# Performance work log

Measured on AMD Instinct MI355X. Metric: run time of the kernel, lower is better.

Reference implementation:

```python
import jax, jax.numpy as jnp
import numpy as np

NEG_BIG = -9e15
ALPHA = 0.2  # LeakyReLU negative slope


def setup_inputs() -> dict:
    key = jax.random.key(0)
    k1, k2, k3, k4 = jax.random.split(key, 4)
    B, N, IN, OUT = 8, 2048, 128, 64
    x = jax.random.normal(k1, (B, N, IN), dtype=jnp.float32)
    adj = jax.random.randint(k2, (B, N, N), 0, 2, dtype=jnp.int32)
    # xavier_uniform with gain=1.414
    lim_W = 1.414 * np.sqrt(6.0 / (IN + OUT))
    W = jax.random.uniform(k3, (IN, OUT), jnp.float32, -lim_W, lim_W)
    lim_a = 1.414 * np.sqrt(6.0 / (2 * OUT + 1))
    a = jax.random.uniform(k4, (2 * OUT, 1), jnp.float32, -lim_a, lim_a)
    return {"x": x, "adj": adj, "W": W, "a": a}


def reference(x, adj, W, a):
    # h: [B, N, out_dim]
    h = jnp.matmul(x, W)
    out_dim = W.shape[1]
    a1 = a[:out_dim, 0]   # applied to h_i (row / destination)
    a2 = a[out_dim:, 0]   # applied to h_j (col / source)
    # e_ij = leakyrelu(h_i . a1 + h_j . a2)  -- avoids the O(B*N*N*2d) concat
    si = jnp.einsum('bnd,d->bn', h, a1)  # [B, N]
    sj = jnp.einsum('bnd,d->bn', h, a2)  # [B, N]
    e = si[:, :, None] + sj[:, None, :]  # [B, N, N]
    e = jnp.where(e > 0, e, ALPHA * e)   # LeakyReLU
    e = jnp.where(adj > 0, e, NEG_BIG)
    attention = jax.nn.softmax(e, axis=-1)  # [B, N, N]
    # dropout p=0.0 (eval mode): identity
    h_prime = jnp.matmul(attention, h)       # [B, N, out_dim]
    return h_prime, attention
```

## Files before the change

### kernel.cpp

```cpp
#include <hip/hip_runtime.h>

#define BB 8
#define NN 2048
#define IND 128
#define OUTD 64
#define ALPHA 0.2f

typedef __attribute__((ext_vector_type(8))) short bf16x8;
typedef __attribute__((ext_vector_type(4))) float f32x4;
typedef unsigned int u32;

__global__ __launch_bounds__(256) void k1_hproj(const float* __restrict__ x,
                                                const float* __restrict__ W,
                                                const float* __restrict__ a,
                                                short* __restrict__ hT_hi,
                                                short* __restrict__ hT_lo,
                                                float* __restrict__ si,
                                                float* __restrict__ sj) {
    __shared__ float Wl[IND * OUTD];
    __shared__ float xl[16][IND];
    __shared__ float tile[16][OUTD + 1];
    int t = threadIdx.x, lane = t & 63, wave = t >> 6;

    const float4* W4 = (const float4*)W;
    float4* Wl4 = (float4*)Wl;
    #pragma unroll
    for (int q = 0; q < 8; ++q) Wl4[t + q * 256] = W4[t + q * 256];

    int row0 = blockIdx.x * 16;
    const float4* x4 = (const float4*)(x + (size_t)row0 * IND);
    float4* xl4 = (float4*)&xl[0][0];
    xl4[t] = x4[t];
    xl4[t + 256] = x4[t + 256];
    __syncthreads();

    float a1v = a[lane];
    float a2v = a[OUTD + lane];

    float acc[4] = {0.f, 0.f, 0.f, 0.f};
    int rbase = wave * 4;
    for (int k = 0; k < IND; k += 4) {
        float4 xv0 = *(const float4*)&xl[rbase + 0][k];
        float4 xv1 = *(const float4*)&xl[rbase + 1][k];
        float4 xv2 = *(const float4*)&xl[rbase + 2][k];
        float4 xv3 = *(const float4*)&xl[rbase + 3][k];
        #pragma unroll
        for (int q = 0; q < 4; ++q) {
            float w = Wl[(k + q) * OUTD + lane];
            acc[0] = fmaf(((const float*)&xv0)[q], w, acc[0]);
            acc[1] = fmaf(((const float*)&xv1)[q], w, acc[1]);
            acc[2] = fmaf(((const float*)&xv2)[q], w, acc[2]);
            acc[3] = fmaf(((const float*)&xv3)[q], w, acc[3]);
        }
    }
    #pragma unroll
    for (int rr = 0; rr < 4; ++rr) {
        size_t grow = (size_t)row0 + rbase + rr;
        tile[rbase + rr][lane] = acc[rr];
        float v1 = acc[rr] * a1v;
        float v2 = acc[rr] * a2v;
        #pragma unroll
        for (int o = 32; o; o >>= 1) {
            v1 += __shfl_xor(v1, o);
            v2 += __shfl_xor(v2, o);
        }
        if (lane == 0) { si[grow] = v1; sj[grow] = v2; }
    }
    __syncthreads();

    int d = t >> 2, kq = (t & 3) * 4;
    int b = row0 >> 11;
    int krow = (row0 & (NN - 1)) + kq;
    float v0 = tile[kq + 0][d], v1 = tile[kq + 1][d];
    float v2 = tile[kq + 2][d], v3 = tile[kq + 3][d];
    u32 b0 = __float_as_uint(v0), b1 = __float_as_uint(v1);
    u32 b2 = __float_as_uint(v2), b3 = __float_as_uint(v3);
    u32 h0 = b0 & 0xffff0000u, h1 = b1 & 0xffff0000u;
    u32 h2 = b2 & 0xffff0000u, h3 = b3 & 0xffff0000u;
    float l0 = v0 - __uint_as_float(h0), l1 = v1 - __uint_as_float(h1);
    float l2 = v2 - __uint_as_float(h2), l3 = v3 - __uint_as_float(h3);
    uint2 hi2, lo2;
    hi2.x = (b0 >> 16) | h1;
    hi2.y = (b2 >> 16) | h3;
    lo2.x = (__float_as_uint(l0) >> 16) | (__float_as_uint(l1) & 0xffff0000u);
    lo2.y = (__float_as_uint(l2) >> 16) | (__float_as_uint(l3) & 0xffff0000u);
    size_t off = ((size_t)b * OUTD + d) * NN + krow;
    *(uint2*)(hT_hi + off) = hi2;
    *(uint2*)(hT_lo + off) = lo2;
}

__global__ __launch_bounds__(256) void k2_mask(const int* __restrict__ adj,
                                               const float* __restrict__ si,
                                               const float* __restrict__ sj,
                                               float* __restrict__ invS,
                                               unsigned char* __restrict__ mask) {
    int t = threadIdx.x, lane = t & 63, w = t >> 6;
    int row = blockIdx.x * 4 + w;
    int b = row >> 11;
    float s_i = si[row];
    const int4* arow = (const int4*)(adj + (size_t)row * NN);
    const float* sjb = sj + (size_t)b * NN;

    float sum = 0.f;
    #pragma unroll
    for (int q = 0; q < 8; ++q) {
        int4 av = arow[q * 64 + lane];
        float4 sv = *(const float4*)(sjb + q * 256 + lane * 4);
        unsigned nib = 0;
        float e, pe;
        e = s_i + sv.x; e = e > 0.f ? e : ALPHA * e; pe = __expf(e);
        if (av.x > 0) { nib |= 1u; sum += pe; }
        e = s_i + sv.y; e = e > 0.f ? e : ALPHA * e; pe = __expf(e);
        if (av.y > 0) { nib |= 2u; sum += pe; }
        e = s_i + sv.z; e = e > 0.f ? e : ALPHA * e; pe = __expf(e);
        if (av.z > 0) { nib |= 4u; sum += pe; }
        e = s_i + sv.w; e = e > 0.f ? e : ALPHA * e; pe = __expf(e);
        if (av.w > 0) { nib |= 8u; sum += pe; }
        unsigned pn = (unsigned)__shfl_xor((int)nib, 1);
        if (!(lane & 1))
            mask[(size_t)row * 256 + q * 32 + (lane >> 1)] = (unsigned char)(nib | (pn << 4));
    }
    #pragma unroll
    for (int o = 32; o; o >>= 1) sum += __shfl_xor(sum, o);
    if (lane == 0) invS[row] = sum > 0.f ? 1.0f / sum : 0.f;
}

__global__ __launch_bounds__(256) void k3_attn_pv(const unsigned char* __restrict__ mask,
                                                  const float* __restrict__ si,
                                                  const float* __restrict__ sj,
                                                  const float* __restrict__ invS,
                                                  const short* __restrict__ hT_hi,
                                                  const short* __restrict__ hT_lo,
                                                  float* __restrict__ attn,
                                                  float* __restrict__ hp) {
    __shared__ float si_s[16], inv_s[16];
    __shared__ f32x4 red[4][4][64];

    int t = threadIdx.x, lane = t & 63, w = t >> 6;
    int bk = blockIdx.x;
    int b = bk >> 7;
    int i0 = (bk & 127) * 16;
    size_t rowbase = (size_t)b * NN + i0;
    const float* sjb = sj + (size_t)b * NN;

    if (t < 16) {
        si_s[t] = si[rowbase + t];
        inv_s[t] = invS[rowbase + t];
    }
    __syncthreads();

    #pragma unroll 4
    for (int it = 0; it < 32; ++it) {
        int idx = it * 256 + t;
        int row = idx >> 9;
        int col = (idx & 511) << 2;
        float4 sv = *(const float4*)(sjb + col);
        unsigned char mb = mask[(rowbase + row) * 256 + (col >> 3)];
        unsigned nib = (mb >> (col & 4)) & 0xFu;
        float s_i = si_s[row], inv = inv_s[row];
        float4 pv;
        float e;
        e = s_i + sv.x; e = e > 0.f ? e : ALPHA * e;
        pv.x = (nib & 1u) ? __expf(e) * inv : 0.f;
        e = s_i + sv.y; e = e > 0.f ? e : ALPHA * e;
        pv.y = (nib & 2u) ? __expf(e) * inv : 0.f;
        e = s_i + sv.z; e = e > 0.f ? e : ALPHA * e;
        pv.z = (nib & 4u) ? __expf(e) * inv : 0.f;
        e = s_i + sv.w; e = e > 0.f ? e : ALPHA * e;
        pv.w = (nib & 8u) ? __expf(e) * inv : 0.f;
        *(float4*)(attn + (rowbase + row) * (size_t)NN + col) = pv;
    }

    int m = lane & 15, g = lane >> 4;
    float si_m = si_s[m];
    float inv_m = inv_s[m];
    const short* bh_base = hT_hi + ((size_t)b * OUTD + m) * NN;
    const short* bl_base = hT_lo + ((size_t)b * OUTD + m) * NN;

    f32x4 acc[4];
    #pragma unroll
    for (int tt = 0; tt < 4; ++tt) acc[tt] = (f32x4){0.f, 0.f, 0.f, 0.f};

    for (int step = 0; step < 16; ++step) {
        int jb = w * 512 + step * 32 + g * 8;
        float4 s0 = *(const float4*)(sjb + jb);
        float4 s1 = *(const float4*)(sjb + jb + 4);
        unsigned mb = mask[(rowbase + m) * 256 + (jb >> 3)];
        float sv[8] = {s0.x, s0.y, s0.z, s0.w, s1.x, s1.y, s1.z, s1.w};
        float p[8];
        #pragma unroll
        for (int q = 0; q < 8; ++q) {
            float e = si_m + sv[q];
            e = e > 0.f ? e : ALPHA * e;
            float pe = __expf(e) * inv_m;
            p[q] = ((mb >> q) & 1u) ? pe : 0.f;
        }

        union { bf16x8 v; u32 u[4]; } ph, pl;
        #pragma unroll
        for (int q = 0; q < 4; ++q) {
            u32 c0 = __float_as_uint(p[2 * q]), c1 = __float_as_uint(p[2 * q + 1]);
            u32 t0 = c0 & 0xffff0000u, t1 = c1 & 0xffff0000u;
            float d0 = p[2 * q] - __uint_as_float(t0);
            float d1 = p[2 * q + 1] - __uint_as_float(t1);
            ph.u[q] = (c0 >> 16) | t1;
            pl.u[q] = (__float_as_uint(d0) >> 16) | (__float_as_uint(d1) & 0xffff0000u);
        }

        #pragma unroll
        for (int tt = 0; tt < 4; ++tt) {
            bf16x8 bh = *(const bf16x8*)(bh_base + (size_t)tt * 16 * NN + jb);
            bf16x8 bl = *(const bf16x8*)(bl_base + (size_t)tt * 16 * NN + jb);
            acc[tt] = __builtin_amdgcn_mfma_f32_16x16x32_bf16(ph.v, bh, acc[tt], 0, 0, 0);
            acc[tt] = __builtin_amdgcn_mfma_f32_16x16x32_bf16(ph.v, bl, acc[tt], 0, 0, 0);
            acc[tt] = __builtin_amdgcn_mfma_f32_16x16x32_bf16(pl.v, bh, acc[tt], 0, 0, 0);
        }
    }

    #pragma unroll
    for (int tt = 0; tt < 4; ++tt) red[w][tt][lane] = acc[tt];
    __syncthreads();

    for (int idx = t; idx < 16 * OUTD; idx += 256) {
        int row = idx >> 6, n = idx & 63;
        int ln = (row >> 2) * 16 + (n & 15);
        int reg = row & 3;
        float v = ((const float*)&red[0][n >> 4][ln])[reg]
                + ((const float*)&red[1][n >> 4][ln])[reg]
                + ((const float*)&red[2][n >> 4][ln])[reg]
                + ((const float*)&red[3][n >> 4][ln])[reg];
        hp[(rowbase + row) * OUTD + n] = v;
    }
}

extern "C" void kernel_launch(void* const* d_in, const int* in_sizes, int n_in,
                              void* d_out, int out_size, void* d_ws, size_t ws_size,
                              hipStream_t stream) {
    const float* x   = (const float*)d_in[0];
    const int*   adj = (const int*)d_in[1];
    const float* W   = (const float*)d_in[2];
    const float* a   = (const float*)d_in[3];

    float* out  = (float*)d_out;
    float* hp   = out;
    float* attn = out + (size_t)BB * NN * OUTD;

    char* ws = (char*)d_ws;
    short* hT_hi = (short*)ws;
    short* hT_lo = hT_hi + (size_t)BB * OUTD * NN;
    float* si    = (float*)(hT_lo + (size_t)BB * OUTD * NN);
    float* sj    = si + (size_t)BB * NN;
    float* invS  = sj + (size_t)BB * NN;
    unsigned char* mask = (unsigned char*)(invS + (size_t)BB * NN);

    k1_hproj<<<BB * NN / 16, 256, 0, stream>>>(x, W, a, hT_hi, hT_lo, si, sj);
    k2_mask<<<BB * NN / 4, 256, 0, stream>>>(adj, si, sj, invS, mask);
    k3_attn_pv<<<BB * NN / 16, 256, 0, stream>>>(mask, si, sj, invS, hT_hi, hT_lo, attn, hp);
}
```

Before: 156.1 us.

## Fuse mask/row-sum kernel into attention kernel with LDS-resident bitmask

Merges the adjacency-mask and softmax-denominator kernel into the attention/PV kernel. Each 512-thread block builds its 16-row bitmask and inverse sums in LDS, so the global mask and invS round trip and one launch go away. Attention writes now use nontemporal stores, and the PV loop is split across 8 waves instead of 4, with an 8-way LDS reduction. The risk is lower occupancy from the larger blocks and more LDS, plus less overlap between the adj read and the attention write within a block.

```diff
diff --git a/kernel.cpp b/kernel.cpp
--- a/kernel.cpp
+++ b/kernel.cpp
@@ -89,52 +89,16 @@
     *(uint2*)(hT_lo + off) = lo2;
 }
 
-__global__ __launch_bounds__(256) void k2_mask(const int* __restrict__ adj,
-                                               const float* __restrict__ si,
-                                               const float* __restrict__ sj,
-                                               float* __restrict__ invS,
-                                               unsigned char* __restrict__ mask) {
-    int t = threadIdx.x, lane = t & 63, w = t >> 6;
-    int row = blockIdx.x * 4 + w;
-    int b = row >> 11;
-    float s_i = si[row];
-    const int4* arow = (const int4*)(adj + (size_t)row * NN);
-    const float* sjb = sj + (size_t)b * NN;
-
-    float sum = 0.f;
-    #pragma unroll
-    for (int q = 0; q < 8; ++q) {
-        int4 av = arow[q * 64 + lane];
-        float4 sv = *(const float4*)(sjb + q * 256 + lane * 4);
-        unsigned nib = 0;
-        float e, pe;
-        e = s_i + sv.x; e = e > 0.f ? e : ALPHA * e; pe = __expf(e);
-        if (av.x > 0) { nib |= 1u; sum += pe; }
-        e = s_i + sv.y; e = e > 0.f ? e : ALPHA * e; pe = __expf(e);
-        if (av.y > 0) { nib |= 2u; sum += pe; }
-        e = s_i + sv.z; e = e > 0.f ? e : ALPHA * e; pe = __expf(e);
-        if (av.z > 0) { nib |= 4u; sum += pe; }
-        e = s_i + sv.w; e = e > 0.f ? e : ALPHA * e; pe = __expf(e);
-        if (av.w > 0) { nib |= 8u; sum += pe; }
-        unsigned pn = (unsigned)__shfl_xor((int)nib, 1);
-        if (!(lane & 1))
-            mask[(size_t)row * 256 + q * 32 + (lane >> 1)] = (unsigned char)(nib | (pn << 4));
-    }
-    #pragma unroll
-    for (int o = 32; o; o >>= 1) sum += __shfl_xor(sum, o);
-    if (lane == 0) invS[row] = sum > 0.f ? 1.0f / sum : 0.f;
-}
-
-__global__ __launch_bounds__(256) void k3_attn_pv(const unsigned char* __restrict__ mask,
-                                                  const float* __restrict__ si,
-                                                  const float* __restrict__ sj,
-                                                  const float* __restrict__ invS,
-                                                  const short* __restrict__ hT_hi,
-                                                  const short* __restrict__ hT_lo,
-                                                  float* __restrict__ attn,
-                                                  float* __restrict__ hp) {
-    __shared__ float si_s[16], inv_s[16];
-    __shared__ f32x4 red[4][4][64];
+__global__ __launch_bounds__(512) void k23(const int* __restrict__ adj,
+                                           const float* __restrict__ si,
+                                           const float* __restrict__ sj,
+                                           const short* __restrict__ hT_hi,
+                                           const short* __restrict__ hT_lo,
+                                           float* __restrict__ attn,
+                                           float* __restrict__ hp) {
+    __shared__ unsigned char mask_lds[16][264];
+    __shared__ float si_lds[16], inv_lds[16];
+    __shared__ f32x4 red[8][4][64];
 
     int t = threadIdx.x, lane = t & 63, w = t >> 6;
     int bk = blockIdx.x;
@@ -142,38 +106,68 @@
     int i0 = (bk & 127) * 16;
     size_t rowbase = (size_t)b * NN + i0;
     const float* sjb = sj + (size_t)b * NN;
-
-    if (t < 16) {
-        si_s[t] = si[rowbase + t];
-        inv_s[t] = invS[rowbase + t];
-    }
-    __syncthreads();
-
-    #pragma unroll 4
-    for (int it = 0; it < 32; ++it) {
-        int idx = it * 256 + t;
-        int row = idx >> 9;
-        int col = (idx & 511) << 2;
-        float4 sv = *(const float4*)(sjb + col);
-        unsigned char mb = mask[(rowbase + row) * 256 + (col >> 3)];
-        unsigned nib = (mb >> (col & 4)) & 0xFu;
-        float s_i = si_s[row], inv = inv_s[row];
-        float4 pv;
-        float e;
-        e = s_i + sv.x; e = e > 0.f ? e : ALPHA * e;
-        pv.x = (nib & 1u) ? __expf(e) * inv : 0.f;
-        e = s_i + sv.y; e = e > 0.f ? e : ALPHA * e;
-        pv.y = (nib & 2u) ? __expf(e) * inv : 0.f;
-        e = s_i + sv.z; e = e > 0.f ? e : ALPHA * e;
-        pv.z = (nib & 4u) ? __expf(e) * inv : 0.f;
-        e = s_i + sv.w; e = e > 0.f ? e : ALPHA * e;
-        pv.w = (nib & 8u) ? __expf(e) * inv : 0.f;
-        *(float4*)(attn + (rowbase + row) * (size_t)NN + col) = pv;
+    const f32x4* sjb4 = (const f32x4*)sjb;
+
+    #pragma unroll
+    for (int rr = 0; rr < 2; ++rr) {
+        int row = w * 2 + rr;
+        size_t grow = rowbase + row;
+        float s_i = si[grow];
+        const int4* arow = (const int4*)(adj + grow * NN);
+        float sum = 0.f;
+        #pragma unroll
+        for (int q = 0; q < 8; ++q) {
+            int4 av = arow[q * 64 + lane];
+            f32x4 sv = sjb4[q * 64 + lane];
+            unsigned nib = 0;
+            float e, pe;
+            e = s_i + sv.x; e = e > 0.f ? e : ALPHA * e; pe = __expf(e);
+            if (av.x > 0) { nib |= 1u; sum += pe; }
+            e = s_i + sv.y; e = e > 0.f ? e : ALPHA * e; pe = __expf(e);
+            if (av.y > 0) { nib |= 2u; sum += pe; }
+            e = s_i + sv.z; e = e > 0.f ? e : ALPHA * e; pe = __expf(e);
+            if (av.z > 0) { nib |= 4u; sum += pe; }
+            e = s_i + sv.w; e = e > 0.f ? e : ALPHA * e; pe = __expf(e);
+            if (av.w > 0) { nib |= 8u; sum += pe; }
+            unsigned pn = (unsigned)__shfl_xor((int)nib, 1);
+            if (!(lane & 1))
+                mask_lds[row][q * 32 + (lane >> 1)] = (unsigned char)(nib | (pn << 4));
+        }
+        #pragma unroll
+        for (int o = 32; o; o >>= 1) sum += __shfl_xor(sum, o);
+        if (lane == 0) {
+            si_lds[row] = s_i;
+            inv_lds[row] = sum > 0.f ? 1.0f / sum : 0.f;
+        }
+    }
+    __syncthreads();
+
+    {
+        f32x4 sv = sjb4[t];
+        int mbyte = t >> 1;
+        int nshift = (t & 1) * 4;
+        #pragma unroll 4
+        for (int row = 0; row < 16; ++row) {
+            unsigned nib = ((unsigned)mask_lds[row][mbyte] >> nshift) & 0xFu;
+            float s_i = si_lds[row], inv = inv_lds[row];
+            f32x4 pv;
+            float e;
+            e = s_i + sv.x; e = e > 0.f ? e : ALPHA * e;
+            pv.x = (nib & 1u) ? __expf(e) * inv : 0.f;
+            e = s_i + sv.y; e = e > 0.f ? e : ALPHA * e;
+            pv.y = (nib & 2u) ? __expf(e) * inv : 0.f;
+            e = s_i + sv.z; e = e > 0.f ? e : ALPHA * e;
+            pv.z = (nib & 4u) ? __expf(e) * inv : 0.f;
+            e = s_i + sv.w; e = e > 0.f ? e : ALPHA * e;
+            pv.w = (nib & 8u) ? __expf(e) * inv : 0.f;
+            __builtin_nontemporal_store(pv,
+                (f32x4*)(attn + (rowbase + row) * (size_t)NN + (size_t)t * 4));
+        }
     }
 
     int m = lane & 15, g = lane >> 4;
-    float si_m = si_s[m];
-    float inv_m = inv_s[m];
+    float si_m = si_lds[m];
+    float inv_m = inv_lds[m];
     const short* bh_base = hT_hi + ((size_t)b * OUTD + m) * NN;
     const short* bl_base = hT_lo + ((size_t)b * OUTD + m) * NN;
 
@@ -181,11 +175,11 @@
     #pragma unroll
     for (int tt = 0; tt < 4; ++tt) acc[tt] = (f32x4){0.f, 0.f, 0.f, 0.f};
 
-    for (int step = 0; step < 16; ++step) {
-        int jb = w * 512 + step * 32 + g * 8;
-        float4 s0 = *(const float4*)(sjb + jb);
-        float4 s1 = *(const float4*)(sjb + jb + 4);
-        unsigned mb = mask[(rowbase + m) * 256 + (jb >> 3)];
+    for (int step = 0; step < 8; ++step) {
+        int jb = w * 256 + step * 32 + g * 8;
+        f32x4 s0 = *(const f32x4*)(sjb + jb);
+        f32x4 s1 = *(const f32x4*)(sjb + jb + 4);
+        unsigned mb = mask_lds[m][jb >> 3];
         float sv[8] = {s0.x, s0.y, s0.z, s0.w, s1.x, s1.y, s1.z, s1.w};
         float p[8];
         #pragma unroll
@@ -221,14 +215,15 @@
     for (int tt = 0; tt < 4; ++tt) red[w][tt][lane] = acc[tt];
     __syncthreads();
 
-    for (int idx = t; idx < 16 * OUTD; idx += 256) {
+    #pragma unroll
+    for (int idx = t; idx < 16 * OUTD; idx += 512) {
         int row = idx >> 6, n = idx & 63;
         int ln = (row >> 2) * 16 + (n & 15);
         int reg = row & 3;
-        float v = ((const float*)&red[0][n >> 4][ln])[reg]
-                + ((const float*)&red[1][n >> 4][ln])[reg]
-                + ((const float*)&red[2][n >> 4][ln])[reg]
-                + ((const float*)&red[3][n >> 4][ln])[reg];
+        float v = 0.f;
+        #pragma unroll
+        for (int ww = 0; ww < 8; ++ww)
+            v += ((const float*)&red[ww][n >> 4][ln])[reg];
         hp[(rowbase + row) * OUTD + n] = v;
     }
 }
@@ -250,10 +245,7 @@
     short* hT_lo = hT_hi + (size_t)BB * OUTD * NN;
     float* si    = (float*)(hT_lo + (size_t)BB * OUTD * NN);
     float* sj    = si + (size_t)BB * NN;
-    float* invS  = sj + (size_t)BB * NN;
-    unsigned char* mask = (unsigned char*)(invS + (size_t)BB * NN);
 
     k1_hproj<<<BB * NN / 16, 256, 0, stream>>>(x, W, a, hT_hi, hT_lo, si, sj);
-    k2_mask<<<BB * NN / 4, 256, 0, stream>>>(adj, si, sj, invS, mask);
-    k3_attn_pv<<<BB * NN / 16, 256, 0, stream>>>(mask, si, sj, invS, hT_hi, hT_lo, attn, hp);
+    k23<<<BB * NN / 16, 512, 0, stream>>>(adj, si, sj, hT_hi, hT_lo, attn, hp);
 }
```

New measurement: 124.9 us. 20.0% less time.

## Split attention write and PV matmul into separate kernels

Applied to the files above, without the earlier changes.

Moves the attention-matrix write out of the fused attention/PV kernel into a dedicated streaming kernel in which each wave writes two full rows. The PV MFMA kernel now reads si/invS directly and unrolls its step loop by two. The aim is to separate the store-bandwidth-bound attention write from the compute-bound PV work so each can be scheduled on its own. In exchange the exponentials are computed twice and there is one more kernel launch.

```diff
diff --git a/kernel.cpp b/kernel.cpp
--- a/kernel.cpp
+++ b/kernel.cpp
@@ -99,13 +99,13 @@
     int b = row >> 11;
     float s_i = si[row];
     const int4* arow = (const int4*)(adj + (size_t)row * NN);
-    const float* sjb = sj + (size_t)b * NN;
+    const f32x4* sjb4 = (const f32x4*)(sj + (size_t)b * NN);
 
     float sum = 0.f;
     #pragma unroll
     for (int q = 0; q < 8; ++q) {
         int4 av = arow[q * 64 + lane];
-        float4 sv = *(const float4*)(sjb + q * 256 + lane * 4);
+        f32x4 sv = sjb4[q * 64 + lane];
         unsigned nib = 0;
         float e, pe;
         e = s_i + sv.x; e = e > 0.f ? e : ALPHA * e; pe = __expf(e);
@@ -125,15 +125,51 @@
     if (lane == 0) invS[row] = sum > 0.f ? 1.0f / sum : 0.f;
 }
 
-__global__ __launch_bounds__(256) void k3_attn_pv(const unsigned char* __restrict__ mask,
-                                                  const float* __restrict__ si,
-                                                  const float* __restrict__ sj,
-                                                  const float* __restrict__ invS,
-                                                  const short* __restrict__ hT_hi,
-                                                  const short* __restrict__ hT_lo,
-                                                  float* __restrict__ attn,
-                                                  float* __restrict__ hp) {
-    __shared__ float si_s[16], inv_s[16];
+__global__ __launch_bounds__(256) void k3_attn(const unsigned char* __restrict__ mask,
+                                               const float* __restrict__ si,
+                                               const float* __restrict__ sj,
+                                               const float* __restrict__ invS,
+                                               float* __restrict__ attn) {
+    int t = threadIdx.x, lane = t & 63, w = t >> 6;
+    int wrow = (blockIdx.x * 4 + w) * 2;
+
+    #pragma unroll
+    for (int r = 0; r < 2; ++r) {
+        int row = wrow + r;
+        int b = row >> 11;
+        float s_i = si[row];
+        float inv = invS[row];
+        const f32x4* sjb4 = (const f32x4*)(sj + (size_t)b * NN);
+        const unsigned char* mrow = mask + (size_t)row * 256;
+        float* arow = attn + (size_t)row * NN;
+
+        #pragma unroll
+        for (int q = 0; q < 8; ++q) {
+            f32x4 sv = sjb4[q * 64 + lane];
+            unsigned mb = mrow[q * 32 + (lane >> 1)];
+            unsigned nib = (mb >> ((lane & 1) * 4)) & 0xFu;
+            f32x4 pv;
+            float e;
+            e = s_i + sv.x; e = e > 0.f ? e : ALPHA * e;
+            pv.x = (nib & 1u) ? __expf(e) * inv : 0.f;
+            e = s_i + sv.y; e = e > 0.f ? e : ALPHA * e;
+            pv.y = (nib & 2u) ? __expf(e) * inv : 0.f;
+            e = s_i + sv.z; e = e > 0.f ? e : ALPHA * e;
+            pv.z = (nib & 4u) ? __expf(e) * inv : 0.f;
+            e = s_i + sv.w; e = e > 0.f ? e : ALPHA * e;
+            pv.w = (nib & 8u) ? __expf(e) * inv : 0.f;
+            *(f32x4*)(arow + q * 256 + lane * 4) = pv;
+        }
+    }
+}
+
+__global__ __launch_bounds__(256) void k4_pv(const unsigned char* __restrict__ mask,
+                                             const float* __restrict__ si,
+                                             const float* __restrict__ sj,
+                                             const float* __restrict__ invS,
+                                             const short* __restrict__ hT_hi,
+                                             const short* __restrict__ hT_lo,
+                                             float* __restrict__ hp) {
     __shared__ f32x4 red[4][4][64];
 
     int t = threadIdx.x, lane = t & 63, w = t >> 6;
@@ -143,49 +179,24 @@
     size_t rowbase = (size_t)b * NN + i0;
     const float* sjb = sj + (size_t)b * NN;
 
-    if (t < 16) {
-        si_s[t] = si[rowbase + t];
-        inv_s[t] = invS[rowbase + t];
-    }
-    __syncthreads();
-
-    #pragma unroll 4
-    for (int it = 0; it < 32; ++it) {
-        int idx = it * 256 + t;
-        int row = idx >> 9;
-        int col = (idx & 511) << 2;
-        float4 sv = *(const float4*)(sjb + col);
-        unsigned char mb = mask[(rowbase + row) * 256 + (col >> 3)];
-        unsigned nib = (mb >> (col & 4)) & 0xFu;
-        float s_i = si_s[row], inv = inv_s[row];
-        float4 pv;
-        float e;
-        e = s_i + sv.x; e = e > 0.f ? e : ALPHA * e;
-        pv.x = (nib & 1u) ? __expf(e) * inv : 0.f;
-        e = s_i + sv.y; e = e > 0.f ? e : ALPHA * e;
-        pv.y = (nib & 2u) ? __expf(e) * inv : 0.f;
-        e = s_i + sv.z; e = e > 0.f ? e : ALPHA * e;
-        pv.z = (nib & 4u) ? __expf(e) * inv : 0.f;
-        e = s_i + sv.w; e = e > 0.f ? e : ALPHA * e;
-        pv.w = (nib & 8u) ? __expf(e) * inv : 0.f;
-        *(float4*)(attn + (rowbase + row) * (size_t)NN + col) = pv;
-    }
-
     int m = lane & 15, g = lane >> 4;
-    float si_m = si_s[m];
-    float inv_m = inv_s[m];
-    const short* bh_base = hT_hi + ((size_t)b * OUTD + m) * NN;
-    const short* bl_base = hT_lo + ((size_t)b * OUTD + m) * NN;
+    float si_m = si[rowbase + m];
+    float inv_m = invS[rowbase + m];
+    const unsigned char* mrow = mask + (rowbase + m) * 256;
+    const short* bh0 = hT_hi + ((size_t)b * OUTD + m) * NN;
+    const short* bl0 = hT_lo + ((size_t)b * OUTD + m) * NN;
 
     f32x4 acc[4];
     #pragma unroll
     for (int tt = 0; tt < 4; ++tt) acc[tt] = (f32x4){0.f, 0.f, 0.f, 0.f};
 
+    #pragma unroll 2
     for (int step = 0; step < 16; ++step) {
-        int jb = w * 512 + step * 32 + g * 8;
-        float4 s0 = *(const float4*)(sjb + jb);
-        float4 s1 = *(const float4*)(sjb + jb + 4);
-        unsigned mb = mask[(rowbase + m) * 256 + (jb >> 3)];
+        int kk = w * 512 + step * 32;
+        int c0 = kk + g * 8;
+        unsigned mb = mrow[(kk >> 3) + g];
+        f32x4 s0 = *(const f32x4*)(sjb + c0);
+        f32x4 s1 = *(const f32x4*)(sjb + c0 + 4);
         float sv[8] = {s0.x, s0.y, s0.z, s0.w, s1.x, s1.y, s1.z, s1.w};
         float p[8];
         #pragma unroll
@@ -199,18 +210,18 @@
         union { bf16x8 v; u32 u[4]; } ph, pl;
         #pragma unroll
         for (int q = 0; q < 4; ++q) {
-            u32 c0 = __float_as_uint(p[2 * q]), c1 = __float_as_uint(p[2 * q + 1]);
-            u32 t0 = c0 & 0xffff0000u, t1 = c1 & 0xffff0000u;
+            u32 c0u = __float_as_uint(p[2 * q]), c1u = __float_as_uint(p[2 * q + 1]);
+            u32 t0 = c0u & 0xffff0000u, t1 = c1u & 0xffff0000u;
             float d0 = p[2 * q] - __uint_as_float(t0);
             float d1 = p[2 * q + 1] - __uint_as_float(t1);
-            ph.u[q] = (c0 >> 16) | t1;
+            ph.u[q] = (c0u >> 16) | t1;
             pl.u[q] = (__float_as_uint(d0) >> 16) | (__float_as_uint(d1) & 0xffff0000u);
         }
 
         #pragma unroll
         for (int tt = 0; tt < 4; ++tt) {
-            bf16x8 bh = *(const bf16x8*)(bh_base + (size_t)tt * 16 * NN + jb);
-            bf16x8 bl = *(const bf16x8*)(bl_base + (size_t)tt * 16 * NN + jb);
+            bf16x8 bh = *(const bf16x8*)(bh0 + (size_t)tt * 16 * NN + c0);
+            bf16x8 bl = *(const bf16x8*)(bl0 + (size_t)tt * 16 * NN + c0);
             acc[tt] = __builtin_amdgcn_mfma_f32_16x16x32_bf16(ph.v, bh, acc[tt], 0, 0, 0);
             acc[tt] = __builtin_amdgcn_mfma_f32_16x16x32_bf16(ph.v, bl, acc[tt], 0, 0, 0);
             acc[tt] = __builtin_amdgcn_mfma_f32_16x16x32_bf16(pl.v, bh, acc[tt], 0, 0, 0);
@@ -255,5 +266,6 @@
 
     k1_hproj<<<BB * NN / 16, 256, 0, stream>>>(x, W, a, hT_hi, hT_lo, si, sj);
     k2_mask<<<BB * NN / 4, 256, 0, stream>>>(adj, si, sj, invS, mask);
-    k3_attn_pv<<<BB * NN / 16, 256, 0, stream>>>(mask, si, sj, invS, hT_hi, hT_lo, attn, hp);
-}
+    k3_attn<<<BB * NN / 8, 256, 0, stream>>>(mask, si, sj, invS, attn);
+    k4_pv<<<BB * NN / 16, 256, 0, stream>>>(mask, si, sj, invS, hT_hi, hT_lo, hp);
+}
```

After: 158.2 us. About the same (+1.4%).
